# Kernel tuning notes

Measured on AMD Instinct MI355X. Metric: run time of the kernel, lower is better.

## Reference

```python
import jax, jax.numpy as jnp
import numpy as np

WS = 8
SHIFT = 4
HEADS = 12
LOG2_8 = np.log2(8.0)
EPS = 1e-12


def _layernorm(x, g, b):
    m = jnp.mean(x, axis=-1, keepdims=True)
    v = jnp.var(x, axis=-1, keepdims=True)
    return (x - m) / jnp.sqrt(v + 1e-5) * g + b


def _rel_position_index(ws):
    coords = np.stack(np.meshgrid(np.arange(ws), np.arange(ws), indexing='ij'))  # (2,ws,ws)
    cf = coords.reshape(2, -1)
    rel = cf[:, :, None] - cf[:, None, :]            # (2,N,N)
    rel = rel.transpose(1, 2, 0)                      # (N,N,2)
    rel[:, :, 0] += ws - 1
    rel[:, :, 1] += ws - 1
    rel[:, :, 0] *= 2 * ws - 1
    return rel.sum(-1)                                # (N,N) int


def _cpb_coords_table(ws):
    r = np.arange(-(ws - 1), ws, dtype=np.float32)
    t = np.stack(np.meshgrid(r, r, indexing='ij')).transpose(1, 2, 0).reshape(-1, 2)
    t /= max(ws - 1, 1)
    t *= 8.0
    return (np.sign(t) * np.log2(np.abs(t) + 1.0) / LOG2_8).astype(np.float32)  # ((2ws-1)^2,2)


def _shift_mask(Hp, Wp, ws, ss):
    img = np.zeros((Hp, Wp), dtype=np.float32)
    cnt = 0
    for h in (slice(0, -ws), slice(-ws, -ss), slice(-ss, None)):
        for w in (slice(0, -ws), slice(-ws, -ss), slice(-ss, None)):
            img[h, w] = cnt
            cnt += 1
    mw = img.reshape(Hp // ws, ws, Wp // ws, ws).transpose(0, 2, 1, 3).reshape(-1, ws * ws)
    diff = mw[:, None, :] - mw[:, :, None]           # (nW,N,N)
    return np.where(diff != 0, -np.inf, 0.0).astype(np.float32)


def _window_partition(x, ws):
    B, H, W, C = x.shape
    x = x.reshape(B, H // ws, ws, W // ws, ws, C)
    return x.transpose(0, 1, 3, 2, 4, 5).reshape(-1, ws * ws, C)


def _window_reverse(wins, ws, B, H, W):
    C = wins.shape[-1]
    x = wins.reshape(B, H // ws, W // ws, ws, ws, C)
    return x.transpose(0, 1, 3, 2, 4, 5).reshape(B, H, W, C)


def reference(x, H, W, norm1_g, norm1_b, qkv_w, qkv_b, proj_w, proj_b,
              cpb_w1, cpb_b1, cpb_w2, logit_scale, norm2_g, norm2_b,
              w12_w, w12_b, w3_w, w3_b):
    B, L, C = x.shape
    ws, ss, nh = WS, SHIFT, HEADS
    hd = C // nh
    N = ws * ws

    shortcut = x
    xn = _layernorm(x, norm1_g, norm1_b).reshape(B, H, W, C)
    # H,W divisible by ws -> no padding
    shifted = jnp.roll(xn, (-ss, -ss), axis=(1, 2))
    xw = _window_partition(shifted, ws)               # (B_, N, C)
    B_ = xw.shape[0]

    # QKV
    qkv = (xw @ qkv_w.T + qkv_b).reshape(B_, N, 3, nh, hd).transpose(2, 0, 3, 1, 4)
    q, k, v = qkv[0], qkv[1], qkv[2]                  # (B_, h, N, hd)

    # cosine attention
    q = q / jnp.maximum(jnp.linalg.norm(q, axis=-1, keepdims=True), EPS)
    k = k / jnp.maximum(jnp.linalg.norm(k, axis=-1, keepdims=True), EPS)
    ls = jnp.exp(jnp.minimum(logit_scale, jnp.log(1.0 / 0.01)))  # (h,1,1)
    q = q * ls[None]

    # CPB relative position bias
    table = jnp.asarray(_cpb_coords_table(ws))        # ((2ws-1)^2, 2)
    bias_table = jax.nn.relu(table @ cpb_w1.T + cpb_b1) @ cpb_w2.T   # ((2ws-1)^2, h)
    rpi = jnp.asarray(_rel_position_index(ws))        # (N,N)
    bias = bias_table[rpi.reshape(-1)].reshape(N, N, nh).transpose(2, 0, 1)  # (h,N,N)

    mask = jnp.asarray(_shift_mask(H, W, ws, ss))     # (nW,N,N)
    nW = mask.shape[0]
    attn = jnp.einsum('bhnd,bhmd->bhnm', q, k)        # (B_,h,N,N)
    attn = attn + bias[None] + jnp.tile(mask, (B_ // nW, 1, 1))[:, None]
    attn = jax.nn.softmax(attn, axis=-1)
    out = jnp.einsum('bhnm,bhmd->bhnd', attn, v)      # (B_,h,N,hd)
    out = out.transpose(0, 2, 1, 3).reshape(B_, N, C)
    out = out @ proj_w.T + proj_b

    shifted = _window_reverse(out, ws, B, H, W)
    xo = jnp.roll(shifted, (ss, ss), axis=(1, 2)).reshape(B, L, C)
    x = shortcut + xo

    # SwiGLU FFN
    h12 = _layernorm(x, norm2_g, norm2_b) @ w12_w.T + w12_b
    x1, x2 = jnp.split(h12, 2, axis=-1)
    ffn = (jax.nn.silu(x2) * x1) @ w3_w.T + w3_b
    return x + ffn


def setup_inputs():
    key = jax.random.key(0)
    ks = jax.random.split(key, 8)
    C, hid, nh = 384, 1536, 12
    s = lambda d: 1.0 / np.sqrt(d)
    return {
        'x': jax.random.normal(ks[0], (32, 4096, C), jnp.float32),
        'H': 64, 'W': 64,
        'norm1_g': jnp.ones((C,), jnp.float32),
        'norm1_b': jnp.zeros((C,), jnp.float32),
        'qkv_w': jax.random.normal(ks[1], (3 * C, C), jnp.float32) * s(C),
        'qkv_b': jnp.zeros((3 * C,), jnp.float32),
        'proj_w': jax.random.normal(ks[2], (C, C), jnp.float32) * s(C),
        'proj_b': jnp.zeros((C,), jnp.float32),
        'cpb_w1': jax.random.normal(ks[3], (512, 2), jnp.float32) * s(2),
        'cpb_b1': jnp.zeros((512,), jnp.float32),
        'cpb_w2': jax.random.normal(ks[4], (nh, 512), jnp.float32) * s(512),
        'logit_scale': jnp.full((nh, 1, 1), np.log(10.0), jnp.float32),
        'norm2_g': jnp.ones((C,), jnp.float32),
        'norm2_b': jnp.zeros((C,), jnp.float32),
        'w12_w': jax.random.normal(ks[5], (2 * hid, C), jnp.float32) * s(C),
        'w12_b': jnp.zeros((2 * hid,), jnp.float32),
        'w3_w': jax.random.normal(ks[6], (C, hid), jnp.float32) * s(hid),
        'w3_b': jnp.zeros((C,), jnp.float32),
    }
```

## Files before the change

kernel.cpp:

```cpp
#include <hip/hip_runtime.h>
#include <hip/hip_bf16.h>
#include <stdint.h>


typedef __attribute__((ext_vector_type(8))) short bf16x8;
typedef __attribute__((ext_vector_type(4))) float f32x4;

__device__ __forceinline__ float bf2f(unsigned int u) {
  unsigned int v = u << 16;
  float f;
  __builtin_memcpy(&f, &v, 4);
  return f;
}
__device__ __forceinline__ unsigned short f2bf(float f) {
  unsigned int x;
  __builtin_memcpy(&x, &f, 4);
  unsigned int r = x + 0x7fffu + ((x >> 16) & 1u);
  return (unsigned short)(r >> 16);
}

__device__ __forceinline__ void gload16(const unsigned short* g, short* l) {
  __builtin_amdgcn_global_load_lds((const __attribute__((address_space(1))) char*)g,
                                   (__attribute__((address_space(3))) char*)l,
                                   16, 0, 0);
}


__global__ void cvt_bf16_kernel(const float* __restrict__ in,
                                unsigned short* __restrict__ out, int n) {
  int i = blockIdx.x * 256 + threadIdx.x;
  if (i < n) out[i] = f2bf(in[i]);
}

__global__ void w12_reorder_kernel(const float* __restrict__ in,
                                   unsigned short* __restrict__ out) {
  int i = blockIdx.x * 256 + threadIdx.x;
  int n = i / 384, k = i - n * 384;
  int g = n >> 4, m = n & 15;
  int src = (g & 1) ? (1536 + (g >> 1) * 16 + m) : ((g >> 1) * 16 + m);
  out[i] = f2bf(in[src * 384 + k]);
}

__global__ void cpb_table_kernel(const float* __restrict__ w1,
                                 const float* __restrict__ b1,
                                 const float* __restrict__ w2,
                                 float* __restrict__ tbl) {
  int r = threadIdx.x;
  if (r >= 225) return;
  int a = r / 15, c = r - a * 15;
  float fy = (float)(a - 7) * (8.0f / 7.0f);
  float fx = (float)(c - 7) * (8.0f / 7.0f);
  float sy = (fy > 0.f) ? 1.f : ((fy < 0.f) ? -1.f : 0.f);
  float sx = (fx > 0.f) ? 1.f : ((fx < 0.f) ? -1.f : 0.f);
  float t0 = sy * log2f(fabsf(fy) + 1.f) * (1.0f / 3.0f);
  float t1 = sx * log2f(fabsf(fx) + 1.f) * (1.0f / 3.0f);
  float acc[12];
#pragma unroll
  for (int h = 0; h < 12; ++h) acc[h] = 0.f;
  for (int j = 0; j < 512; ++j) {
    float hj = w1[j * 2] * t0 + w1[j * 2 + 1] * t1 + b1[j];
    hj = fmaxf(hj, 0.f);
#pragma unroll
    for (int h = 0; h < 12; ++h) acc[h] += w2[h * 512 + j] * hj;
  }
#pragma unroll
  for (int h = 0; h < 12; ++h) tbl[r * 12 + h] = acc[h];
}

__global__ void bias_fill_kernel(const float* __restrict__ tbl,
                                 float* __restrict__ bias) {
  int idx = blockIdx.x * 256 + threadIdx.x;
  int h = idx >> 12, ij = idx & 4095;
  int i = ij >> 6, j = ij & 63;
  int dy = (i >> 3) - (j >> 3) + 7;
  int dx = (i & 7) - (j & 7) + 7;
  bias[idx] = tbl[(dy * 15 + dx) * 12 + h];
}

__global__ __launch_bounds__(256) void ln_kernel(const float* __restrict__ xin,
                                                 const float* __restrict__ g,
                                                 const float* __restrict__ b,
                                                 unsigned short* __restrict__ outw,
                                                 int shift_mode) {
  int wid = threadIdx.x >> 6, lane = threadIdx.x & 63;
  int t = blockIdx.x * 4 + wid;
  const float* xp = xin + (size_t)t * 384;
  float v[6];
  float s = 0.f, sq = 0.f;
#pragma unroll
  for (int i = 0; i < 6; ++i) {
    v[i] = xp[lane + i * 64];
    s += v[i];
    sq += v[i] * v[i];
  }
#pragma unroll
  for (int off = 32; off >= 1; off >>= 1) {
    s += __shfl_xor(s, off);
    sq += __shfl_xor(sq, off);
  }
  float mean = s * (1.f / 384.f);
  float var = sq * (1.f / 384.f) - mean * mean;
  float rstd = rsqrtf(var + 1e-5f);
  int row;
  if (shift_mode) {
    int bb = t >> 12, rem = t & 4095;
    int hh = rem >> 6, ww = rem & 63;
    int hs = (hh + 60) & 63, wsd = (ww + 60) & 63;
    row = bb * 4096 + ((hs >> 3) * 8 + (wsd >> 3)) * 64 + (hs & 7) * 8 + (wsd & 7);
  } else {
    row = t;
  }
  unsigned short* op = outw + (size_t)row * 384;
#pragma unroll
  for (int i = 0; i < 6; ++i) {
    int c = lane + i * 64;
    op[c] = f2bf((v[i] - mean) * rstd * g[c] + b[c]);
  }
}

template <int MODE>
__global__ __launch_bounds__(256, 2) void gemm_bt(
    const unsigned short* __restrict__ A, const unsigned short* __restrict__ B,
    const float* __restrict__ cbias, unsigned short* __restrict__ outB,
    float* __restrict__ outF, const float* __restrict__ shortcut, int N, int K) {
  __shared__ short As[128][64];
  __shared__ short Bs[128][64];
  int tid = threadIdx.x, wid = tid >> 6, lane = tid & 63;
  int tn = blockIdx.x, tm = blockIdx.y;

  const unsigned short* aSrc =
      A + (size_t)(tm * 128 + wid * 32 + (lane >> 3)) * K + (lane & 7) * 8;
  const unsigned short* bSrc =
      B + (size_t)(tn * 128 + wid * 32 + (lane >> 3)) * K + (lane & 7) * 8;

  f32x4 acc[4][4];
#pragma unroll
  for (int a = 0; a < 4; ++a)
#pragma unroll
    for (int b2 = 0; b2 < 4; ++b2) acc[a][b2] = (f32x4){0.f, 0.f, 0.f, 0.f};

  int wm = (wid >> 1) * 64, wn = (wid & 1) * 64;
  int lr = lane & 15, lk = lane >> 4;
  int nk = K >> 6;

  for (int kt = 0; kt < nk; ++kt) {
#pragma unroll
    for (int t = 0; t < 4; ++t) {
      gload16(aSrc + (size_t)(t * 8) * K + kt * 64, &As[wid * 32 + t * 8][0]);
      gload16(bSrc + (size_t)(t * 8) * K + kt * 64, &Bs[wid * 32 + t * 8][0]);
    }
    __syncthreads();
#pragma unroll
    for (int kk = 0; kk < 2; ++kk) {
      bf16x8 af[4], bfr[4];
#pragma unroll
      for (int mi = 0; mi < 4; ++mi)
        af[mi] = *(const bf16x8*)&As[wm + mi * 16 + lr][kk * 32 + lk * 8];
#pragma unroll
      for (int ni = 0; ni < 4; ++ni)
        bfr[ni] = *(const bf16x8*)&Bs[wn + ni * 16 + lr][kk * 32 + lk * 8];
#pragma unroll
      for (int mi = 0; mi < 4; ++mi)
#pragma unroll
        for (int ni = 0; ni < 4; ++ni)
          acc[mi][ni] =
              __builtin_amdgcn_mfma_f32_16x16x32_bf16(af[mi], bfr[ni], acc[mi][ni], 0, 0, 0);
    }
    __syncthreads();
  }

  int row0 = tm * 128 + wm + lk * 4;
  int col0 = tn * 128 + wn + lr;
#pragma unroll
  for (int mi = 0; mi < 4; ++mi) {
    if (MODE == 2) {
#pragma unroll
      for (int ni = 0; ni < 4; ni += 2) {
        int colE = col0 + ni * 16;
        int hidx = ((colE >> 5) << 4) + lr;
        float b1v = cbias[hidx];
        float b2v = cbias[1536 + hidx];
#pragma unroll
        for (int reg = 0; reg < 4; ++reg) {
          int row = row0 + mi * 16 + reg;
          float x1 = acc[mi][ni][reg] + b1v;
          float x2 = acc[mi][ni + 1][reg] + b2v;
          float hv = x1 * x2 / (1.f + __expf(-x2));
          outB[(size_t)row * 1536 + hidx] = f2bf(hv);
        }
      }
    } else {
#pragma unroll
      for (int ni = 0; ni < 4; ++ni) {
        int col = col0 + ni * 16;
        float bv = cbias[col];
#pragma unroll
        for (int reg = 0; reg < 4; ++reg) {
          int row = row0 + mi * 16 + reg;
          float v = acc[mi][ni][reg] + bv;
          if (MODE == 0) {
            outB[(size_t)row * N + col] = f2bf(v);
          } else if (MODE == 1) {
            int win = row >> 6, n = row & 63;
            int bb = win >> 6, wd = win & 63;
            int hh = (((wd >> 3) << 3) + (n >> 3) + 4) & 63;
            int ww2 = (((wd & 7) << 3) + (n & 7) + 4) & 63;
            size_t idx = ((size_t)(bb << 12) + hh * 64 + ww2) * 384 + col;
            outF[idx] = v + shortcut[idx];
          } else {
            size_t idx = (size_t)row * 384 + col;
            outF[idx] = v + outF[idx];
          }
        }
      }
    }
  }
}

__global__ __launch_bounds__(256) void attn_kernel(
    const unsigned short* __restrict__ qkv, const float* __restrict__ logit_scale,
    const float* __restrict__ bias, unsigned short* __restrict__ outw) {
  __shared__ float qs[64][33];
  __shared__ float ks[64][33];
  __shared__ float vs[64][33];
  __shared__ float S[64][65];
  int head = blockIdx.x, win = blockIdx.y;
  int tid = threadIdx.x;
  int r = tid >> 2, d0 = (tid & 3) << 3;

  {
    const unsigned short* bp = qkv + (size_t)(win * 64 + r) * 1152 + head * 32 + d0;
    uint4 uq = *(const uint4*)(bp);
    uint4 uk = *(const uint4*)(bp + 384);
    uint4 uv = *(const uint4*)(bp + 768);
    unsigned int aq[4] = {uq.x, uq.y, uq.z, uq.w};
    unsigned int ak[4] = {uk.x, uk.y, uk.z, uk.w};
    unsigned int av[4] = {uv.x, uv.y, uv.z, uv.w};
#pragma unroll
    for (int e = 0; e < 4; ++e) {
      qs[r][d0 + 2 * e] = bf2f(aq[e] & 0xffffu);
      qs[r][d0 + 2 * e + 1] = bf2f(aq[e] >> 16);
      ks[r][d0 + 2 * e] = bf2f(ak[e] & 0xffffu);
      ks[r][d0 + 2 * e + 1] = bf2f(ak[e] >> 16);
      vs[r][d0 + 2 * e] = bf2f(av[e] & 0xffffu);
      vs[r][d0 + 2 * e + 1] = bf2f(av[e] >> 16);
    }
  }
  __syncthreads();

  if (tid < 128) {
    int rr = tid & 63;
    float* arr = (tid < 64) ? qs[rr] : ks[rr];
    float ssum = 0.f;
#pragma unroll
    for (int d = 0; d < 32; ++d) ssum += arr[d] * arr[d];
    float sc = 1.f / fmaxf(sqrtf(ssum), 1e-12f);
    if (tid < 64) sc *= __expf(fminf(logit_scale[head], 4.6051702f));
#pragma unroll
    for (int d = 0; d < 32; ++d) arr[d] *= sc;
  }
  __syncthreads();

  int i = tid >> 2, jg = tid & 3;
  int wd = win & 63, wh = wd >> 3, ww = wd & 7;
  int hi = (wh << 3) + (i >> 3), wi = (ww << 3) + (i & 7);
  int regi = (hi < 56 ? 0 : (hi < 60 ? 1 : 2)) * 3 + (wi < 56 ? 0 : (wi < 60 ? 1 : 2));

  float qf[32];
#pragma unroll
  for (int d = 0; d < 32; ++d) qf[d] = qs[i][d];

  float sv[16];
  const float* bp2 = bias + ((size_t)head * 64 + i) * 64;
#pragma unroll 4
  for (int jj = 0; jj < 16; ++jj) {
    int j = (jg << 4) + jj;
    float dot = 0.f;
#pragma unroll
    for (int d = 0; d < 32; ++d) dot += qf[d] * ks[j][d];
    int hj = (wh << 3) + (j >> 3), wj = (ww << 3) + (j & 7);
    int regj = (hj < 56 ? 0 : (hj < 60 ? 1 : 2)) * 3 + (wj < 56 ? 0 : (wj < 60 ? 1 : 2));
    sv[jj] = dot + bp2[j] + (regi != regj ? -1e30f : 0.f);
  }
  float m = sv[0];
#pragma unroll
  for (int jj = 1; jj < 16; ++jj) m = fmaxf(m, sv[jj]);
  m = fmaxf(m, __shfl_xor(m, 1));
  m = fmaxf(m, __shfl_xor(m, 2));
  float ssum = 0.f;
#pragma unroll
  for (int jj = 0; jj < 16; ++jj) {
    sv[jj] = __expf(sv[jj] - m);
    ssum += sv[jj];
  }
  ssum += __shfl_xor(ssum, 1);
  ssum += __shfl_xor(ssum, 2);
  float inv = 1.f / ssum;
#pragma unroll
  for (int jj = 0; jj < 16; ++jj) S[i][(jg << 4) + jj] = sv[jj] * inv;
  __syncthreads();

  float o[8];
#pragma unroll
  for (int e = 0; e < 8; ++e) o[e] = 0.f;
  for (int j = 0; j < 64; ++j) {
    float p = S[i][j];
#pragma unroll
    for (int e = 0; e < 8; ++e) o[e] += p * vs[j][d0 + e];
  }
  unsigned int p0 = (unsigned)f2bf(o[0]) | ((unsigned)f2bf(o[1]) << 16);
  unsigned int p1 = (unsigned)f2bf(o[2]) | ((unsigned)f2bf(o[3]) << 16);
  unsigned int p2 = (unsigned)f2bf(o[4]) | ((unsigned)f2bf(o[5]) << 16);
  unsigned int p3 = (unsigned)f2bf(o[6]) | ((unsigned)f2bf(o[7]) << 16);
  uint4 u = {p0, p1, p2, p3};
  *(uint4*)&outw[(size_t)(win * 64 + i) * 384 + head * 32 + d0] = u;
}


extern "C" void kernel_launch(void* const* d_in, const int* in_sizes, int n_in,
                              void* d_out, int out_size, void* d_ws, size_t ws_size,
                              hipStream_t stream) {
  const float* x = (const float*)d_in[0];
  const float* n1g = (const float*)d_in[3];
  const float* n1b = (const float*)d_in[4];
  const float* qkv_w = (const float*)d_in[5];
  const float* qkv_b = (const float*)d_in[6];
  const float* proj_w = (const float*)d_in[7];
  const float* proj_b = (const float*)d_in[8];
  const float* cpb_w1 = (const float*)d_in[9];
  const float* cpb_b1 = (const float*)d_in[10];
  const float* cpb_w2 = (const float*)d_in[11];
  const float* lscale = (const float*)d_in[12];
  const float* n2g = (const float*)d_in[13];
  const float* n2b = (const float*)d_in[14];
  const float* w12_w = (const float*)d_in[15];
  const float* w12_b = (const float*)d_in[16];
  const float* w3_w = (const float*)d_in[17];
  const float* w3_b = (const float*)d_in[18];
  float* outF = (float*)d_out;
  char* ws = (char*)d_ws;

  unsigned short* xw = (unsigned short*)(ws + 0ull);
  unsigned short* qkvb = (unsigned short*)(ws + 100663296ull);
  unsigned short* attn = (unsigned short*)(ws + 402653184ull);
  unsigned short* xn2 = attn;
  unsigned short* hbuf = (unsigned short*)(ws + 0ull);
  char* wbase = ws + 503316480ull;
  unsigned short* wqkv = (unsigned short*)(wbase);
  unsigned short* wproj = (unsigned short*)(wbase + 884736ull);
  unsigned short* w12r = (unsigned short*)(wbase + 1179648ull);
  unsigned short* w3b = (unsigned short*)(wbase + 3538944ull);
  float* tbl = (float*)(wbase + 4718592ull);
  float* bias = (float*)(wbase + 4729408ull);

  cvt_bf16_kernel<<<1728, 256, 0, stream>>>(qkv_w, wqkv, 442368);
  cvt_bf16_kernel<<<576, 256, 0, stream>>>(proj_w, wproj, 147456);
  cvt_bf16_kernel<<<2304, 256, 0, stream>>>(w3_w, w3b, 589824);
  w12_reorder_kernel<<<4608, 256, 0, stream>>>(w12_w, w12r);
  cpb_table_kernel<<<1, 256, 0, stream>>>(cpb_w1, cpb_b1, cpb_w2, tbl);
  bias_fill_kernel<<<192, 256, 0, stream>>>(tbl, bias);

  ln_kernel<<<32768, 256, 0, stream>>>(x, n1g, n1b, xw, 1);
  gemm_bt<0><<<dim3(9, 1024), 256, 0, stream>>>(xw, wqkv, qkv_b, qkvb, nullptr, nullptr,
                                                1152, 384);
  attn_kernel<<<dim3(12, 2048), 256, 0, stream>>>(qkvb, lscale, bias, attn);
  gemm_bt<1><<<dim3(3, 1024), 256, 0, stream>>>(attn, wproj, proj_b, nullptr, outF, x,
                                                384, 384);
  ln_kernel<<<32768, 256, 0, stream>>>(outF, n2g, n2b, xn2, 0);
  gemm_bt<2><<<dim3(24, 1024), 256, 0, stream>>>(xn2, w12r, w12_b, hbuf, nullptr, nullptr,
                                                 3072, 384);
  gemm_bt<3><<<dim3(3, 1024), 256, 0, stream>>>(hbuf, w3b, w3_b, nullptr, outF, nullptr,
                                                384, 1536);
}
```

Measured before the change: 2.050 ms.

## Rewrite window attention with bf16 MFMA, one head per wavefront, transposed V

New measurement: 1.739 ms. -15.2%, faster.

```diff
diff --git a/kernel.cpp b/kernel.cpp
--- a/kernel.cpp
+++ b/kernel.cpp
@@ -17,6 +17,11 @@
   __builtin_memcpy(&x, &f, 4);
   unsigned int r = x + 0x7fffu + ((x >> 16) & 1u);
   return (unsigned short)(r >> 16);
+}
+__device__ __forceinline__ bf16x8 as_bf(uint4 u) {
+  bf16x8 b;
+  __builtin_memcpy(&b, &u, 16);
+  return b;
 }
 
 __device__ __forceinline__ void gload16(const unsigned short* g, short* l) {
@@ -68,13 +73,16 @@
 }
 
 __global__ void bias_fill_kernel(const float* __restrict__ tbl,
-                                 float* __restrict__ bias) {
+                                 float* __restrict__ biasr) {
   int idx = blockIdx.x * 256 + threadIdx.x;
-  int h = idx >> 12, ij = idx & 4095;
-  int i = ij >> 6, j = ij & 63;
+  int head = idx >> 12, rem = idx & 4095;
+  int lane = rem >> 6, q = rem & 63;
+  int fn = q >> 4, fm = (q >> 2) & 3, r = q & 3;
+  int i = (lane & 15) + 16 * fn;
+  int j = ((lane >> 4) << 2) + r + 16 * fm;
   int dy = (i >> 3) - (j >> 3) + 7;
   int dx = (i & 7) - (j & 7) + 7;
-  bias[idx] = tbl[(dy * 15 + dx) * 12 + h];
+  biasr[idx] = tbl[(dy * 15 + dx) * 12 + head];
 }
 
 __global__ __launch_bounds__(256) void ln_kernel(const float* __restrict__ xin,
@@ -122,7 +130,8 @@
 __global__ __launch_bounds__(256, 2) void gemm_bt(
     const unsigned short* __restrict__ A, const unsigned short* __restrict__ B,
     const float* __restrict__ cbias, unsigned short* __restrict__ outB,
-    float* __restrict__ outF, const float* __restrict__ shortcut, int N, int K) {
+    unsigned short* __restrict__ outB2, float* __restrict__ outF,
+    const float* __restrict__ shortcut, int N, int K) {
   __shared__ short As[128][64];
   __shared__ short Bs[128][64];
   int tid = threadIdx.x, wid = tid >> 6, lane = tid & 63;
@@ -189,18 +198,38 @@
           outB[(size_t)row * 1536 + hidx] = f2bf(hv);
         }
       }
-    } else {
+    } else if (MODE == 0) {
 #pragma unroll
       for (int ni = 0; ni < 4; ++ni) {
         int col = col0 + ni * 16;
         float bv = cbias[col];
+        float vals[4];
+#pragma unroll
+        for (int reg = 0; reg < 4; ++reg) vals[reg] = acc[mi][ni][reg] + bv;
+        if (col < 768) {
+#pragma unroll
+          for (int reg = 0; reg < 4; ++reg)
+            outB[(size_t)(row0 + mi * 16 + reg) * 768 + col] = f2bf(vals[reg]);
+        } else {
+          int head = (col >> 5) - 24, d = col & 31;
+          int row = row0 + mi * 16;
+          int win = row >> 6, n0 = row & 63;
+          uint2 p;
+          p.x = (unsigned)f2bf(vals[0]) | ((unsigned)f2bf(vals[1]) << 16);
+          p.y = (unsigned)f2bf(vals[2]) | ((unsigned)f2bf(vals[3]) << 16);
+          *(uint2*)&outB2[((size_t)(head * 2048 + win) * 32 + d) * 64 + n0] = p;
+        }
+      }
+    } else {
+#pragma unroll
+      for (int ni = 0; ni < 4; ++ni) {
+        int col = col0 + ni * 16;
+        float bv = cbias[col];
 #pragma unroll
         for (int reg = 0; reg < 4; ++reg) {
           int row = row0 + mi * 16 + reg;
           float v = acc[mi][ni][reg] + bv;
-          if (MODE == 0) {
-            outB[(size_t)row * N + col] = f2bf(v);
-          } else if (MODE == 1) {
+          if (MODE == 1) {
             int win = row >> 6, n = row & 63;
             int bb = win >> 6, wd = win & 63;
             int hh = (((wd >> 3) << 3) + (n >> 3) + 4) & 63;
@@ -217,103 +246,180 @@
   }
 }
 
-__global__ __launch_bounds__(256) void attn_kernel(
-    const unsigned short* __restrict__ qkv, const float* __restrict__ logit_scale,
-    const float* __restrict__ bias, unsigned short* __restrict__ outw) {
-  __shared__ float qs[64][33];
-  __shared__ float ks[64][33];
-  __shared__ float vs[64][33];
-  __shared__ float S[64][65];
-  int head = blockIdx.x, win = blockIdx.y;
-  int tid = threadIdx.x;
-  int r = tid >> 2, d0 = (tid & 3) << 3;
-
-  {
-    const unsigned short* bp = qkv + (size_t)(win * 64 + r) * 1152 + head * 32 + d0;
-    uint4 uq = *(const uint4*)(bp);
-    uint4 uk = *(const uint4*)(bp + 384);
-    uint4 uv = *(const uint4*)(bp + 768);
-    unsigned int aq[4] = {uq.x, uq.y, uq.z, uq.w};
-    unsigned int ak[4] = {uk.x, uk.y, uk.z, uk.w};
-    unsigned int av[4] = {uv.x, uv.y, uv.z, uv.w};
+__device__ __forceinline__ int zone6(int wd, int z) {
+  int h = ((wd >> 3) << 3) + (z >> 3);
+  int w = ((wd & 7) << 3) + (z & 7);
+  return (h < 56 ? 0 : (h < 60 ? 1 : 2)) * 3 + (w < 56 ? 0 : (w < 60 ? 1 : 2));
+}
+
+__global__ __launch_bounds__(256, 2) void attn2_kernel(
+    const unsigned short* __restrict__ qk,
+    const unsigned short* __restrict__ vt,
+    const float* __restrict__ logit_scale,
+    const float* __restrict__ biasr,
+    unsigned short* __restrict__ outw) {
+  __shared__ __align__(16) char smem[4 * 8704];
+  int wv = threadIdx.x >> 6, lane = threadIdx.x & 63;
+  int head = blockIdx.x * 4 + wv;
+  int win = blockIdx.y;
+  char* Pb = smem + wv * 8704;
+  int li = lane & 15, lg = lane >> 4;
+
+  const unsigned short* qbase = qk + (size_t)(win * 64) * 768 + head * 32 + lg * 8;
+  uint4 qf[4], kf[4];
+#pragma unroll
+  for (int f = 0; f < 4; ++f) {
+    qf[f] = *(const uint4*)(qbase + (size_t)(li + 16 * f) * 768);
+    kf[f] = *(const uint4*)(qbase + 384 + (size_t)(li + 16 * f) * 768);
+  }
+  const unsigned short* vbase = vt + (size_t)(head * 2048 + win) * 2048;
+  uint4 vf[2][2];
+#pragma unroll
+  for (int fm = 0; fm < 2; ++fm)
+#pragma unroll
+    for (int fk = 0; fk < 2; ++fk)
+      vf[fm][fk] = *(const uint4*)(vbase + (size_t)(li + 16 * fm) * 64 + lg * 8 + 32 * fk);
+
+  float rq[4], rk[4];
+#pragma unroll
+  for (int f = 0; f < 4; ++f) {
+    unsigned int aq[4] = {qf[f].x, qf[f].y, qf[f].z, qf[f].w};
+    unsigned int ak[4] = {kf[f].x, kf[f].y, kf[f].z, kf[f].w};
+    float sq = 0.f, sk = 0.f;
 #pragma unroll
     for (int e = 0; e < 4; ++e) {
-      qs[r][d0 + 2 * e] = bf2f(aq[e] & 0xffffu);
-      qs[r][d0 + 2 * e + 1] = bf2f(aq[e] >> 16);
-      ks[r][d0 + 2 * e] = bf2f(ak[e] & 0xffffu);
-      ks[r][d0 + 2 * e + 1] = bf2f(ak[e] >> 16);
-      vs[r][d0 + 2 * e] = bf2f(av[e] & 0xffffu);
-      vs[r][d0 + 2 * e + 1] = bf2f(av[e] >> 16);
-    }
-  }
-  __syncthreads();
-
-  if (tid < 128) {
-    int rr = tid & 63;
-    float* arr = (tid < 64) ? qs[rr] : ks[rr];
-    float ssum = 0.f;
-#pragma unroll
-    for (int d = 0; d < 32; ++d) ssum += arr[d] * arr[d];
-    float sc = 1.f / fmaxf(sqrtf(ssum), 1e-12f);
-    if (tid < 64) sc *= __expf(fminf(logit_scale[head], 4.6051702f));
-#pragma unroll
-    for (int d = 0; d < 32; ++d) arr[d] *= sc;
-  }
-  __syncthreads();
-
-  int i = tid >> 2, jg = tid & 3;
-  int wd = win & 63, wh = wd >> 3, ww = wd & 7;
-  int hi = (wh << 3) + (i >> 3), wi = (ww << 3) + (i & 7);
-  int regi = (hi < 56 ? 0 : (hi < 60 ? 1 : 2)) * 3 + (wi < 56 ? 0 : (wi < 60 ? 1 : 2));
-
-  float qf[32];
-#pragma unroll
-  for (int d = 0; d < 32; ++d) qf[d] = qs[i][d];
-
-  float sv[16];
-  const float* bp2 = bias + ((size_t)head * 64 + i) * 64;
-#pragma unroll 4
-  for (int jj = 0; jj < 16; ++jj) {
-    int j = (jg << 4) + jj;
-    float dot = 0.f;
-#pragma unroll
-    for (int d = 0; d < 32; ++d) dot += qf[d] * ks[j][d];
-    int hj = (wh << 3) + (j >> 3), wj = (ww << 3) + (j & 7);
-    int regj = (hj < 56 ? 0 : (hj < 60 ? 1 : 2)) * 3 + (wj < 56 ? 0 : (wj < 60 ? 1 : 2));
-    sv[jj] = dot + bp2[j] + (regi != regj ? -1e30f : 0.f);
-  }
-  float m = sv[0];
-#pragma unroll
-  for (int jj = 1; jj < 16; ++jj) m = fmaxf(m, sv[jj]);
-  m = fmaxf(m, __shfl_xor(m, 1));
-  m = fmaxf(m, __shfl_xor(m, 2));
-  float ssum = 0.f;
-#pragma unroll
-  for (int jj = 0; jj < 16; ++jj) {
-    sv[jj] = __expf(sv[jj] - m);
-    ssum += sv[jj];
-  }
-  ssum += __shfl_xor(ssum, 1);
-  ssum += __shfl_xor(ssum, 2);
-  float inv = 1.f / ssum;
-#pragma unroll
-  for (int jj = 0; jj < 16; ++jj) S[i][(jg << 4) + jj] = sv[jj] * inv;
-  __syncthreads();
-
-  float o[8];
-#pragma unroll
-  for (int e = 0; e < 8; ++e) o[e] = 0.f;
-  for (int j = 0; j < 64; ++j) {
-    float p = S[i][j];
-#pragma unroll
-    for (int e = 0; e < 8; ++e) o[e] += p * vs[j][d0 + e];
-  }
-  unsigned int p0 = (unsigned)f2bf(o[0]) | ((unsigned)f2bf(o[1]) << 16);
-  unsigned int p1 = (unsigned)f2bf(o[2]) | ((unsigned)f2bf(o[3]) << 16);
-  unsigned int p2 = (unsigned)f2bf(o[4]) | ((unsigned)f2bf(o[5]) << 16);
-  unsigned int p3 = (unsigned)f2bf(o[6]) | ((unsigned)f2bf(o[7]) << 16);
-  uint4 u = {p0, p1, p2, p3};
-  *(uint4*)&outw[(size_t)(win * 64 + i) * 384 + head * 32 + d0] = u;
+      float lo = bf2f(aq[e] & 0xffffu), hi = bf2f(aq[e] >> 16);
+      sq = fmaf(lo, lo, sq);
+      sq = fmaf(hi, hi, sq);
+      lo = bf2f(ak[e] & 0xffffu);
+      hi = bf2f(ak[e] >> 16);
+      sk = fmaf(lo, lo, sk);
+      sk = fmaf(hi, hi, sk);
+    }
+    sq += __shfl_xor(sq, 16);
+    sq += __shfl_xor(sq, 32);
+    sk += __shfl_xor(sk, 16);
+    sk += __shfl_xor(sk, 32);
+    rq[f] = 1.f / fmaxf(sqrtf(sq), 1e-12f);
+    rk[f] = 1.f / fmaxf(sqrtf(sk), 1e-12f);
+  }
+
+  f32x4 accS[4][4];
+#pragma unroll
+  for (int fm = 0; fm < 4; ++fm)
+#pragma unroll
+    for (int fn = 0; fn < 4; ++fn) accS[fm][fn] = (f32x4){0.f, 0.f, 0.f, 0.f};
+#pragma unroll
+  for (int fm = 0; fm < 4; ++fm)
+#pragma unroll
+    for (int fn = 0; fn < 4; ++fn)
+      accS[fm][fn] =
+          __builtin_amdgcn_mfma_f32_16x16x32_bf16(as_bf(kf[fm]), as_bf(qf[fn]), accS[fm][fn], 0, 0, 0);
+
+  float ls = __expf(fminf(logit_scale[head], 4.6051702f));
+  float qsc[4];
+#pragma unroll
+  for (int fn = 0; fn < 4; ++fn) qsc[fn] = ls * rq[fn];
+  f32x4 rkv[4];
+#pragma unroll
+  for (int fm = 0; fm < 4; ++fm)
+#pragma unroll
+    for (int r = 0; r < 4; ++r)
+      rkv[fm][r] = __int_as_float(
+          __builtin_amdgcn_ds_bpermute((lg * 4 + r) << 2, __float_as_int(rk[fm])));
+
+  int wd = win & 63;
+  int regi[4];
+#pragma unroll
+  for (int fn = 0; fn < 4; ++fn) regi[fn] = zone6(wd, li + 16 * fn);
+  const float* bb = biasr + ((size_t)(head * 64 + lane)) * 64;
+  float mx[4] = {-3e38f, -3e38f, -3e38f, -3e38f};
+#pragma unroll
+  for (int fm = 0; fm < 4; ++fm) {
+    int j0 = lg * 4 + 16 * fm;
+    int regj[4];
+#pragma unroll
+    for (int r = 0; r < 4; ++r) regj[r] = zone6(wd, j0 + r);
+#pragma unroll
+    for (int fn = 0; fn < 4; ++fn) {
+      f32x4 bv = *(const f32x4*)(bb + fn * 16 + fm * 4);
+#pragma unroll
+      for (int r = 0; r < 4; ++r) {
+        float val = accS[fm][fn][r] * (qsc[fn] * rkv[fm][r]);
+        val += (regj[r] == regi[fn]) ? bv[r] : -1e30f;
+        accS[fm][fn][r] = val;
+        mx[fn] = fmaxf(mx[fn], val);
+      }
+    }
+  }
+
+  float inv[4];
+#pragma unroll
+  for (int fn = 0; fn < 4; ++fn) {
+    float m = mx[fn];
+    m = fmaxf(m, __shfl_xor(m, 16));
+    m = fmaxf(m, __shfl_xor(m, 32));
+    float sum = 0.f;
+#pragma unroll
+    for (int fm = 0; fm < 4; ++fm)
+#pragma unroll
+      for (int r = 0; r < 4; ++r) {
+        float e = __expf(accS[fm][fn][r] - m);
+        accS[fm][fn][r] = e;
+        sum += e;
+      }
+    sum += __shfl_xor(sum, 16);
+    sum += __shfl_xor(sum, 32);
+    inv[fn] = 1.f / sum;
+  }
+
+#pragma unroll
+  for (int fm = 0; fm < 4; ++fm)
+#pragma unroll
+    for (int fn = 0; fn < 4; ++fn) {
+      uint2 p;
+      p.x = (unsigned)f2bf(accS[fm][fn][0] * inv[fn]) |
+            ((unsigned)f2bf(accS[fm][fn][1] * inv[fn]) << 16);
+      p.y = (unsigned)f2bf(accS[fm][fn][2] * inv[fn]) |
+            ((unsigned)f2bf(accS[fm][fn][3] * inv[fn]) << 16);
+      *(uint2*)(Pb + lane * 136 + fm * 32 + fn * 8) = p;
+    }
+
+  f32x4 accO[2][4];
+#pragma unroll
+  for (int fm = 0; fm < 2; ++fm)
+#pragma unroll
+    for (int fn = 0; fn < 4; ++fn) accO[fm][fn] = (f32x4){0.f, 0.f, 0.f, 0.f};
+
+#pragma unroll
+  for (int fk = 0; fk < 2; ++fk) {
+    bf16x8 pf[4];
+#pragma unroll
+    for (int fn = 0; fn < 4; ++fn) {
+      int s0 = (li + 16 * ((2 * lg) & 3)) * 136 + (2 * fk + (lg >> 1)) * 32 + fn * 8;
+      int s1 = (li + 16 * ((2 * lg + 1) & 3)) * 136 + (2 * fk + (lg >> 1)) * 32 + fn * 8;
+      uint2 x0 = *(const uint2*)(Pb + s0);
+      uint2 x1 = *(const uint2*)(Pb + s1);
+      uint4 comb = {x0.x, x0.y, x1.x, x1.y};
+      pf[fn] = as_bf(comb);
+    }
+#pragma unroll
+    for (int fm = 0; fm < 2; ++fm)
+#pragma unroll
+      for (int fn = 0; fn < 4; ++fn)
+        accO[fm][fn] =
+            __builtin_amdgcn_mfma_f32_16x16x32_bf16(as_bf(vf[fm][fk]), pf[fn], accO[fm][fn], 0, 0, 0);
+  }
+
+#pragma unroll
+  for (int fm = 0; fm < 2; ++fm)
+#pragma unroll
+    for (int fn = 0; fn < 4; ++fn) {
+      uint2 p;
+      p.x = (unsigned)f2bf(accO[fm][fn][0]) | ((unsigned)f2bf(accO[fm][fn][1]) << 16);
+      p.y = (unsigned)f2bf(accO[fm][fn][2]) | ((unsigned)f2bf(accO[fm][fn][3]) << 16);
+      *(uint2*)&outw[(size_t)(win * 64 + li + 16 * fn) * 384 + head * 32 + lg * 4 + 16 * fm] = p;
+    }
 }
 
 
@@ -341,9 +447,10 @@
   char* ws = (char*)d_ws;
 
   unsigned short* xw = (unsigned short*)(ws + 0ull);
-  unsigned short* qkvb = (unsigned short*)(ws + 100663296ull);
-  unsigned short* attn = (unsigned short*)(ws + 402653184ull);
-  unsigned short* xn2 = attn;
+  unsigned short* qkb = (unsigned short*)(ws + 100663296ull);
+  unsigned short* vtb = (unsigned short*)(ws + 301989888ull);
+  unsigned short* attnout = (unsigned short*)(ws + 0ull);
+  unsigned short* xn2 = (unsigned short*)(ws + 402653184ull);
   unsigned short* hbuf = (unsigned short*)(ws + 0ull);
   char* wbase = ws + 503316480ull;
   unsigned short* wqkv = (unsigned short*)(wbase);
@@ -351,24 +458,24 @@
   unsigned short* w12r = (unsigned short*)(wbase + 1179648ull);
   unsigned short* w3b = (unsigned short*)(wbase + 3538944ull);
   float* tbl = (float*)(wbase + 4718592ull);
-  float* bias = (float*)(wbase + 4729408ull);
+  float* biasr = (float*)(wbase + 4729408ull);
 
   cvt_bf16_kernel<<<1728, 256, 0, stream>>>(qkv_w, wqkv, 442368);
   cvt_bf16_kernel<<<576, 256, 0, stream>>>(proj_w, wproj, 147456);
   cvt_bf16_kernel<<<2304, 256, 0, stream>>>(w3_w, w3b, 589824);
   w12_reorder_kernel<<<4608, 256, 0, stream>>>(w12_w, w12r);
   cpb_table_kernel<<<1, 256, 0, stream>>>(cpb_w1, cpb_b1, cpb_w2, tbl);
-  bias_fill_kernel<<<192, 256, 0, stream>>>(tbl, bias);
+  bias_fill_kernel<<<192, 256, 0, stream>>>(tbl, biasr);
 
   ln_kernel<<<32768, 256, 0, stream>>>(x, n1g, n1b, xw, 1);
-  gemm_bt<0><<<dim3(9, 1024), 256, 0, stream>>>(xw, wqkv, qkv_b, qkvb, nullptr, nullptr,
-                                                1152, 384);
-  attn_kernel<<<dim3(12, 2048), 256, 0, stream>>>(qkvb, lscale, bias, attn);
-  gemm_bt<1><<<dim3(3, 1024), 256, 0, stream>>>(attn, wproj, proj_b, nullptr, outF, x,
-                                                384, 384);
+  gemm_bt<0><<<dim3(9, 1024), 256, 0, stream>>>(xw, wqkv, qkv_b, qkb, vtb, nullptr,
+                                                nullptr, 1152, 384);
+  attn2_kernel<<<dim3(3, 2048), 256, 0, stream>>>(qkb, vtb, lscale, biasr, attnout);
+  gemm_bt<1><<<dim3(3, 1024), 256, 0, stream>>>(attnout, wproj, proj_b, nullptr, nullptr,
+                                                outF, x, 384, 384);
   ln_kernel<<<32768, 256, 0, stream>>>(outF, n2g, n2b, xn2, 0);
   gemm_bt<2><<<dim3(24, 1024), 256, 0, stream>>>(xn2, w12r, w12_b, hbuf, nullptr, nullptr,
-                                                 3072, 384);
-  gemm_bt<3><<<dim3(3, 1024), 256, 0, stream>>>(hbuf, w3b, w3_b, nullptr, outF, nullptr,
-                                                384, 1536);
-}
+                                                 nullptr, 3072, 384);
+  gemm_bt<3><<<dim3(3, 1024), 256, 0, stream>>>(hbuf, w3b, w3_b, nullptr, nullptr, outF,
+                                                nullptr, 384, 1536);
+}
```
